# Performance work log

Hardware: AMD Instinct MI355X
Metric: run time of the kernel (lower is better)

Reference implementation:

```python
import jax, jax.numpy as jnp
import numpy as np

WS = 7
B, Dd, Hh, Wd, C, NH = 1, 28, 28, 28, 384, 12

def _rel_index(ws):
    coords = np.stack(np.meshgrid(np.arange(ws), np.arange(ws), np.arange(ws), indexing='ij'))
    cf = coords.reshape(3, -1)
    rel = (cf[:, :, None] - cf[:, None, :]).transpose(1, 2, 0) + (ws - 1)
    rel[:, :, 0] *= (2 * ws - 1) ** 2
    rel[:, :, 1] *= (2 * ws - 1)
    return rel.sum(-1)  # (ws^3, ws^3)

REL_IDX = _rel_index(WS)

def setup_inputs():
    key = jax.random.key(0)
    ks = jax.random.split(key, 8)
    L = Dd * Hh * Wd
    s = 0.02
    return {
        'skip': jax.random.normal(ks[0], (B, L, C), jnp.float32),
        'x_up': jax.random.normal(ks[1], (B, L, C), jnp.float32),
        'D': Dd, 'H': Hh, 'W': Wd,
        'ln1_g': jnp.ones((C,), jnp.float32), 'ln1_b': jnp.zeros((C,), jnp.float32),
        'kv_w': jax.random.normal(ks[2], (C, 2 * C), jnp.float32) * s,
        'kv_b': jnp.zeros((2 * C,), jnp.float32),
        'rpb': jax.random.normal(ks[3], ((2 * WS - 1) ** 3, NH), jnp.float32) * s,
        'proj_w': jax.random.normal(ks[4], (C, C), jnp.float32) * s,
        'proj_b': jnp.zeros((C,), jnp.float32),
        'ln2_g': jnp.ones((C,), jnp.float32), 'ln2_b': jnp.zeros((C,), jnp.float32),
        'mlp_w1': jax.random.normal(ks[5], (C, 4 * C), jnp.float32) * s,
        'mlp_b1': jnp.zeros((4 * C,), jnp.float32),
        'mlp_w2': jax.random.normal(ks[6], (4 * C, C), jnp.float32) * s,
        'mlp_b2': jnp.zeros((C,), jnp.float32),
    }

def _ln(x, g, b):
    m = jnp.mean(x, -1, keepdims=True)
    v = jnp.mean(jnp.square(x - m), -1, keepdims=True)
    return (x - m) * jax.lax.rsqrt(v + 1e-5) * g + b

def _win_part(x):
    b, d, h, w, c = x.shape
    x = x.reshape(b, d // WS, WS, h // WS, WS, w // WS, WS, c)
    return x.transpose(0, 1, 3, 5, 2, 4, 6, 7).reshape(-1, WS ** 3, c)

def _win_rev(x, b, d, h, w):
    c = x.shape[-1]
    x = x.reshape(b, d // WS, h // WS, w // WS, WS, WS, WS, c)
    return x.transpose(0, 1, 4, 2, 5, 3, 6, 7).reshape(b, d, h, w, c)

def reference(skip, x_up, D, H, W, ln1_g, ln1_b, kv_w, kv_b, rpb, proj_w, proj_b, ln2_g, ln2_b, mlp_w1, mlp_b1, mlp_w2, mlp_b2):
    b, L, c = skip.shape
    x = x_up + skip  # wrapper residual; shortcut of the inner block
    # inner block was built with shift_size=0 -> no cyclic shift, attn_mask unused
    sk = _win_part(_ln(skip, ln1_g, ln1_b).reshape(b, D, H, W, c))   # (nW, N, C) -> K,V source
    qx = _win_part(_ln(x_up, ln1_g, ln1_b).reshape(b, D, H, W, c))   # (nW, N, C) -> Q source
    nW, N, _ = sk.shape
    hd = c // NH
    kv = (sk @ kv_w + kv_b).reshape(nW, N, 2, NH, hd)
    k, v = kv[:, :, 0], kv[:, :, 1]                  # (nW, N, NH, hd)
    q = qx.reshape(nW, N, NH, hd) * (hd ** -0.5)     # no q projection in WindowAttention_kv
    attn = jnp.einsum('wqhd,wkhd->whqk', q, k)
    bias = rpb[REL_IDX.reshape(-1)].reshape(N, N, NH).transpose(2, 0, 1)
    attn = jax.nn.softmax(attn + bias[None], axis=-1)
    o = jnp.einsum('whqk,wkhd->wqhd', attn, v).reshape(nW, N, c)
    o = o @ proj_w + proj_b
    o = _win_rev(o, b, D, H, W).reshape(b, L, c)
    x = x + o
    h1 = jax.nn.gelu(_ln(x, ln2_g, ln2_b) @ mlp_w1 + mlp_b1)
    x = x + h1 @ mlp_w2 + mlp_b2
    return x
```

## Files before the change

### kernel.cpp

```cpp
#include <hip/hip_runtime.h>
#include <hip/hip_bf16.h>
#include <cstdint>

typedef unsigned short u16;
typedef short s16x8 __attribute__((ext_vector_type(8)));
typedef short s16x4 __attribute__((ext_vector_type(4)));
typedef float f32x4 __attribute__((ext_vector_type(4)));

#define C_DIM 384
#define NHEAD 12
#define HD    32
#define NTOK  343
#define NWIN  64
#define LTOT  21952
#define SIDE  28

__device__ __forceinline__ float u2f(u16 u) {
    return __uint_as_float(((unsigned int)u) << 16);
}
__device__ __forceinline__ u16 f2b(float f) {
    unsigned int u = __float_as_uint(f);
    return (u16)((u + 0x7fffu + ((u >> 16) & 1u)) >> 16);
}
__device__ __forceinline__ float exp2_hw(float x) {
    float r;
    asm("v_exp_f32 %0, %1" : "=v"(r) : "v"(x));
    return r;
}
__device__ __forceinline__ unsigned int pk_bf16(float lo, float hi) {
    unsigned int r;
    asm("v_cvt_pk_bf16_f32 %0, %1, %2" : "=v"(r) : "v"(lo), "v"(hi));
    return r;
}
__device__ __forceinline__ float gelu_fast(float x) {
    float e = exp2_hw(-2.3022083f * (x + 0.044715f * x * x * x));
    return x * __builtin_amdgcn_rcpf(1.f + e);
}

__global__ __launch_bounds__(256) void k_wt(
    const float* __restrict__ W, u16* __restrict__ Wt, int K, int N)
{
    __shared__ float T[64][65];
    int k0 = blockIdx.x * 64, n0 = blockIdx.y * 64;
    int t = threadIdx.x;
    int c = t & 63, rg = t >> 6;
#pragma unroll
    for (int i = 0; i < 16; i++) {
        int r = rg * 16 + i;
        T[r][c] = W[(size_t)(k0 + r) * N + n0 + c];
    }
    __syncthreads();
    int k = t & 63, ng = t >> 6;
#pragma unroll
    for (int i = 0; i < 16; i++) {
        int n = ng * 16 + i;
        Wt[(size_t)(n0 + n) * K + k0 + k] = f2b(T[k][n]);
    }
}

__global__ __launch_bounds__(256) void k_wt_pi(
    const float* __restrict__ W, u16* __restrict__ Wt, int K, int N)
{
    __shared__ float T[64][65];
    int k0 = blockIdx.x * 64, n0 = blockIdx.y * 64;
    int t = threadIdx.x;
    int c = t & 63, rg = t >> 6;
#pragma unroll
    for (int i = 0; i < 16; i++) {
        int r = rg * 16 + i;
        T[r][c] = W[(size_t)(k0 + r) * N + n0 + c];
    }
    __syncthreads();
    int k = t & 63, ng = t >> 6;
    int kg = k0 + k;
    int j = kg & 127, ct = j >> 4, nn = j & 15;
    int kp = (kg & ~127) | ((ct >> 1) << 5) | (nn << 1) | (ct & 1);
#pragma unroll
    for (int i = 0; i < 16; i++) {
        int n = ng * 16 + i;
        Wt[(size_t)(n0 + n) * K + kp] = f2b(T[k][n]);
    }
}

__global__ __launch_bounds__(256) void k_lnprep(
    const float* __restrict__ skip, const float* __restrict__ xup,
    const float* __restrict__ g, const float* __restrict__ bta,
    u16* __restrict__ skW, u16* __restrict__ qW, u16* __restrict__ res)
{
    int t = blockIdx.x * 4 + (threadIdx.x >> 6);
    int lane = threadIdx.x & 63;
    const float* ps = skip + (size_t)t * C_DIM;
    const float* px = xup + (size_t)t * C_DIM;
    float vs[6], vx[6];
    float s1 = 0.f, s2 = 0.f, x1 = 0.f, x2 = 0.f;
#pragma unroll
    for (int j = 0; j < 6; j++) {
        float a = ps[lane + j * 64];
        float b = px[lane + j * 64];
        vs[j] = a; vx[j] = b;
        s1 += a; s2 += a * a; x1 += b; x2 += b * b;
    }
#pragma unroll
    for (int off = 32; off; off >>= 1) {
        s1 += __shfl_xor(s1, off);
        s2 += __shfl_xor(s2, off);
        x1 += __shfl_xor(x1, off);
        x2 += __shfl_xor(x2, off);
    }
    float ms = s1 * (1.f / 384.f), mx = x1 * (1.f / 384.f);
    float rs = rsqrtf(fmaxf(s2 * (1.f / 384.f) - ms * ms, 0.f) + 1e-5f);
    float rx = rsqrtf(fmaxf(x2 * (1.f / 384.f) - mx * mx, 0.f) + 1e-5f);
    int d = t / 784, rem = t % 784, hh = rem / 28, ww = rem % 28;
    int win = (d / 7) * 16 + (hh / 7) * 4 + (ww / 7);
    int n = (d % 7) * 49 + (hh % 7) * 7 + (ww % 7);
    size_t dst = ((size_t)(win * NTOK + n)) * C_DIM + lane;
    size_t td  = (size_t)t * C_DIM + lane;
#pragma unroll
    for (int j = 0; j < 6; j++) {
        int c = lane + j * 64;
        float gg = g[c], bb = bta[c];
        skW[dst + j * 64] = f2b((vs[j] - ms) * rs * gg + bb);
        qW[dst + j * 64]  = f2b((vx[j] - mx) * rx * gg + bb);
        res[td + j * 64]  = f2b(vs[j] + vx[j]);
    }
}

__global__ __launch_bounds__(256) void k_ln2(
    const u16* __restrict__ x2, const float* __restrict__ g,
    const float* __restrict__ bta, u16* __restrict__ lnx)
{
    int t = blockIdx.x * 4 + (threadIdx.x >> 6);
    int lane = threadIdx.x & 63;
    const u16* p = x2 + (size_t)t * C_DIM;
    float v[6];
    float s1 = 0.f, s2 = 0.f;
#pragma unroll
    for (int j = 0; j < 6; j++) {
        float a = u2f(p[lane + j * 64]);
        v[j] = a; s1 += a; s2 += a * a;
    }
#pragma unroll
    for (int off = 32; off; off >>= 1) {
        s1 += __shfl_xor(s1, off);
        s2 += __shfl_xor(s2, off);
    }
    float m = s1 * (1.f / 384.f);
    float r = rsqrtf(fmaxf(s2 * (1.f / 384.f) - m * m, 0.f) + 1e-5f);
    size_t dst = (size_t)t * C_DIM + lane;
#pragma unroll
    for (int j = 0; j < 6; j++) {
        int c = lane + j * 64;
        lnx[dst + j * 64] = f2b((v[j] - m) * r * g[c] + bta[c]);
    }
}

#define BPAD 40

__device__ __forceinline__ void gemm128(
    const u16* __restrict__ A, const u16* __restrict__ Bt, int K, int M,
    int rowBase, int colBase, int tid,
    u16 (*As)[BPAD], u16 (*Bs)[BPAD], f32x4 acc[2][8])
{
    const int sr  = tid >> 2;
    const int scg = (tid & 3) << 3;
    const int lane = tid & 63, wv = tid >> 6;
    const int m16 = lane & 15, quad = lane >> 4;

    int ra0 = min(rowBase + sr, M - 1);
    int ra1 = min(rowBase + 64 + sr, M - 1);
    const u16* pa0 = A + (size_t)ra0 * K + scg;
    const u16* pa1 = A + (size_t)ra1 * K + scg;
    const u16* pb0 = Bt + (size_t)(colBase + sr) * K + scg;
    const u16* pb1 = Bt + (size_t)(colBase + 64 + sr) * K + scg;

    uint4 a0 = *(const uint4*)pa0, a1 = *(const uint4*)pa1;
    uint4 b0 = *(const uint4*)pb0, b1 = *(const uint4*)pb1;

    for (int kk = 0; kk < K; kk += 32) {
        *(uint4*)&As[sr][scg]      = a0;
        *(uint4*)&As[64 + sr][scg] = a1;
        *(uint4*)&Bs[sr][scg]      = b0;
        *(uint4*)&Bs[64 + sr][scg] = b1;
        __syncthreads();
        if (kk + 32 < K) {
            a0 = *(const uint4*)(pa0 + kk + 32);
            a1 = *(const uint4*)(pa1 + kk + 32);
            b0 = *(const uint4*)(pb0 + kk + 32);
            b1 = *(const uint4*)(pb1 + kk + 32);
        }
        s16x8 af0 = *(const s16x8*)&As[wv * 32 + m16][quad * 8];
        s16x8 af1 = *(const s16x8*)&As[wv * 32 + 16 + m16][quad * 8];
#pragma unroll
        for (int c = 0; c < 8; c++) {
            s16x8 bf = *(const s16x8*)&Bs[c * 16 + m16][quad * 8];
            acc[0][c] = __builtin_amdgcn_mfma_f32_16x16x32_bf16(af0, bf, acc[0][c], 0, 0, 0);
            acc[1][c] = __builtin_amdgcn_mfma_f32_16x16x32_bf16(af1, bf, acc[1][c], 0, 0, 0);
        }
        __syncthreads();
    }
}

__device__ __forceinline__ void gemm64_d2(
    const u16* __restrict__ A, const u16* __restrict__ Bt, int K, int M,
    int rowBase, int colBase, int tid,
    u16 (*As)[BPAD], u16 (*Bs)[BPAD], f32x4 acc[8])
{
    const int sr  = tid >> 2;
    const int scg = (tid & 3) << 3;
    const int lane = tid & 63, wv = tid >> 6;
    const int m16 = lane & 15, quad = lane >> 4;

    int ra = min(rowBase + sr, M - 1);
    const u16* pa  = A + (size_t)ra * K + scg;
    const u16* pb0 = Bt + (size_t)(colBase + sr) * K + scg;
    const u16* pb1 = Bt + (size_t)(colBase + 64 + sr) * K + scg;

    uint4 a0  = *(const uint4*)pa;
    uint4 b00 = *(const uint4*)pb0;
    uint4 b01 = *(const uint4*)pb1;
    uint4 a1  = *(const uint4*)(pa + 32);
    uint4 b10 = *(const uint4*)(pb0 + 32);
    uint4 b11 = *(const uint4*)(pb1 + 32);

    for (int kk = 0; kk < K; kk += 64) {
        *(uint4*)&As[sr][scg]      = a0;
        *(uint4*)&Bs[sr][scg]      = b00;
        *(uint4*)&Bs[64 + sr][scg] = b01;
        __syncthreads();
        if (kk + 64 < K) {
            a0  = *(const uint4*)(pa  + kk + 64);
            b00 = *(const uint4*)(pb0 + kk + 64);
            b01 = *(const uint4*)(pb1 + kk + 64);
        }
        {
            s16x8 af = *(const s16x8*)&As[wv * 16 + m16][quad * 8];
#pragma unroll
            for (int c = 0; c < 8; c++) {
                s16x8 bf = *(const s16x8*)&Bs[c * 16 + m16][quad * 8];
                acc[c] = __builtin_amdgcn_mfma_f32_16x16x32_bf16(af, bf, acc[c], 0, 0, 0);
            }
        }
        __syncthreads();
        *(uint4*)&As[sr][scg]      = a1;
        *(uint4*)&Bs[sr][scg]      = b10;
        *(uint4*)&Bs[64 + sr][scg] = b11;
        __syncthreads();
        if (kk + 96 < K) {
            a1  = *(const uint4*)(pa  + kk + 96);
            b10 = *(const uint4*)(pb0 + kk + 96);
            b11 = *(const uint4*)(pb1 + kk + 96);
        }
        {
            s16x8 af = *(const s16x8*)&As[wv * 16 + m16][quad * 8];
#pragma unroll
            for (int c = 0; c < 8; c++) {
                s16x8 bf = *(const s16x8*)&Bs[c * 16 + m16][quad * 8];
                acc[c] = __builtin_amdgcn_mfma_f32_16x16x32_bf16(af, bf, acc[c], 0, 0, 0);
            }
        }
        __syncthreads();
    }
}

#define EPI_SETUP \
    int lane = tid & 63, wv = tid >> 6, quad = lane >> 4, n16 = lane & 15;

__global__ __launch_bounds__(256) void k_gemm_kv(
    const u16* __restrict__ A, const u16* __restrict__ Wt, const float* __restrict__ bias,
    u16* __restrict__ Kb, u16* __restrict__ Vb)
{
    __shared__ __align__(16) u16 As[128][BPAD];
    __shared__ __align__(16) u16 Bs[128][BPAD];
    f32x4 acc[2][8] = {};
    int tid = threadIdx.x;
    int rowBase = blockIdx.x * 128, colBase = blockIdx.y * 128;
    gemm128(A, Wt, 384, LTOT, rowBase, colBase, tid, As, Bs, acc);
    EPI_SETUP
#pragma unroll
    for (int c = 0; c < 8; c++) {
        int col = colBase + c * 16 + n16;
        float bcol = bias[col];
        int isv = col >= 384;
        int remc = col - (isv ? 384 : 0);
        int hh = remc >> 5, dd = remc & 31;
#pragma unroll
        for (int rt = 0; rt < 2; rt++)
#pragma unroll
        for (int reg = 0; reg < 4; reg++) {
            int r = rowBase + wv * 32 + rt * 16 + quad * 4 + reg;
            if (r < LTOT) {
                int w = r / NTOK, nn = r % NTOK;
                size_t dst = ((size_t)((w * NHEAD + hh) * NTOK + nn)) * HD + dd;
                (isv ? Vb : Kb)[dst] = f2b(acc[rt][c][reg] + bcol);
            }
        }
    }
}

__global__ __launch_bounds__(256) void k_gemm_proj(
    const u16* __restrict__ A, const u16* __restrict__ Wt, const float* __restrict__ bias,
    const u16* __restrict__ res, u16* __restrict__ x2)
{
    __shared__ __align__(16) u16 As[64][BPAD];
    __shared__ __align__(16) u16 Bs[128][BPAD];
    f32x4 acc[8] = {};
    int tid = threadIdx.x;
    int rowBase = blockIdx.x * 64, colBase = blockIdx.y * 128;
    gemm64_d2(A, Wt, 384, LTOT, rowBase, colBase, tid, As, Bs, acc);
    EPI_SETUP
#pragma unroll
    for (int c = 0; c < 8; c++) {
        int col = colBase + c * 16 + n16;
        float bcol = bias[col];
#pragma unroll
        for (int reg = 0; reg < 4; reg++) {
            int r = rowBase + wv * 16 + quad * 4 + reg;
            if (r < LTOT) {
                size_t idx = (size_t)r * C_DIM + col;
                x2[idx] = f2b(acc[c][reg] + bcol + u2f(res[idx]));
            }
        }
    }
}

__global__ __launch_bounds__(256) void k_gemm_mlp1(
    const u16* __restrict__ A, const u16* __restrict__ Wt, const float* __restrict__ bias,
    u16* __restrict__ h1c, int rowOfs)
{
    __shared__ __align__(16) u16 As[128][BPAD];
    __shared__ __align__(16) u16 Bs[128][BPAD];
    f32x4 acc[2][8] = {};
    int tid = threadIdx.x;
    int rowBase = rowOfs + blockIdx.x * 128, colBase = blockIdx.y * 128;
    gemm128(A, Wt, 384, LTOT, rowBase, colBase, tid, As, Bs, acc);
    EPI_SETUP
#pragma unroll
    for (int p = 0; p < 4; p++) {
        int col0 = colBase + p * 32 + n16;
        int col1 = col0 + 16;
        float bc0 = bias[col0], bc1 = bias[col1];
        int dcol = colBase + p * 32 + 2 * n16;
#pragma unroll
        for (int rt = 0; rt < 2; rt++)
#pragma unroll
        for (int reg = 0; reg < 4; reg++) {
            int r = rowBase + wv * 32 + rt * 16 + quad * 4 + reg;
            if (r < LTOT) {
                size_t rl = (size_t)(r - rowOfs);
                float v0 = gelu_fast(acc[rt][2 * p][reg] + bc0);
                float v1 = gelu_fast(acc[rt][2 * p + 1][reg] + bc1);
                *(unsigned int*)&h1c[rl * 1536 + dcol] = pk_bf16(v0, v1);
            }
        }
    }
}

__global__ __launch_bounds__(256) void k_gemm_mlp2(
    const u16* __restrict__ A, const u16* __restrict__ Wt, const float* __restrict__ bias,
    const u16* __restrict__ x2, float* __restrict__ out, int rowOfs, int chunkRows)
{
    __shared__ __align__(16) u16 As[64][BPAD];
    __shared__ __align__(16) u16 Bs[128][BPAD];
    f32x4 acc[8] = {};
    int tid = threadIdx.x;
    int rowBase = blockIdx.x * 64, colBase = blockIdx.y * 128;
    gemm64_d2(A, Wt, 1536, chunkRows, rowBase, colBase, tid, As, Bs, acc);
    EPI_SETUP
#pragma unroll
    for (int c = 0; c < 8; c++) {
        int col = colBase + c * 16 + n16;
        float bcol = bias[col];
#pragma unroll
        for (int reg = 0; reg < 4; reg++) {
            int rl = rowBase + wv * 16 + quad * 4 + reg;
            int rg = rowOfs + rl;
            if (rl < chunkRows && rg < LTOT) {
                size_t idx = (size_t)rg * C_DIM + col;
                out[idx] = acc[c][reg] + bcol + u2f(x2[idx]);
            }
        }
    }
}

#define KP  40
#define VP  360
#define PBS 36

__global__ __launch_bounds__(256, 2) void k_attn(
    const u16* __restrict__ qW, const u16* __restrict__ Kb, const u16* __restrict__ Vb,
    const float* __restrict__ rpb, u16* __restrict__ oT)
{
    __shared__ __align__(16) u16 Ks[352 * KP];
    __shared__ __align__(16) u16 Vt[32 * VP];
    __shared__ __align__(16) u16 rp16[2200];
    __shared__ __align__(16) u16 code[352];
    __shared__ __align__(16) u16 Pb[4 * 16 * PBS];

    const int h = blockIdx.x, w = blockIdx.y;
    const int tid = threadIdx.x;
    const int lane = tid & 63, wv = tid >> 6;
    const int m16 = lane & 15, quad = lane >> 4;
    const size_t base = ((size_t)(w * NHEAD + h)) * NTOK * HD;

    for (int t = tid; t < 1408; t += 256) {
        int r = t >> 2, c = (t & 3) << 3;
        uint4 u = make_uint4(0, 0, 0, 0);
        if (r < NTOK) u = *(const uint4*)(Kb + base + r * HD + c);
        *(uint4*)&Ks[r * KP + c] = u;
    }
    for (int t = tid; t < 704; t += 256) {
        int dg = t / 176, rem = t - dg * 176;
        int kb = rem >> 4, j = rem & 15;
        int n0 = kb * 32 + j, n1 = n0 + 16;
        uint4 uA = make_uint4(0, 0, 0, 0), uB = make_uint4(0, 0, 0, 0);
        if (n0 < NTOK) uA = *(const uint4*)(Vb + base + n0 * HD + dg * 8);
        if (n1 < NTOK) uB = *(const uint4*)(Vb + base + n1 * HD + dg * 8);
        int d0 = dg * 8, colu = kb * 32 + 2 * j;
        unsigned int pk0 = (uA.x & 0xffffu) | (uB.x << 16);
        unsigned int pk1 = (uA.x >> 16)     | (uB.x & 0xffff0000u);
        unsigned int pk2 = (uA.y & 0xffffu) | (uB.y << 16);
        unsigned int pk3 = (uA.y >> 16)     | (uB.y & 0xffff0000u);
        unsigned int pk4 = (uA.z & 0xffffu) | (uB.z << 16);
        unsigned int pk5 = (uA.z >> 16)     | (uB.z & 0xffff0000u);
        unsigned int pk6 = (uA.w & 0xffffu) | (uB.w << 16);
        unsigned int pk7 = (uA.w >> 16)     | (uB.w & 0xffff0000u);
        *(unsigned int*)&Vt[(d0 + 0) * VP + colu] = pk0;
        *(unsigned int*)&Vt[(d0 + 1) * VP + colu] = pk1;
        *(unsigned int*)&Vt[(d0 + 2) * VP + colu] = pk2;
        *(unsigned int*)&Vt[(d0 + 3) * VP + colu] = pk3;
        *(unsigned int*)&Vt[(d0 + 4) * VP + colu] = pk4;
        *(unsigned int*)&Vt[(d0 + 5) * VP + colu] = pk5;
        *(unsigned int*)&Vt[(d0 + 6) * VP + colu] = pk6;
        *(unsigned int*)&Vt[(d0 + 7) * VP + colu] = pk7;
    }
    for (int t = tid; t < 2200; t += 256)
        rp16[t] = (t < 2197) ? f2b(rpb[t * NHEAD + h] * 1.4426950408889634f) : (u16)0;
    for (int t = tid; t < 352; t += 256) {
        int z = t / 49, rem = t % 49, y = rem / 7, x = rem % 7;
        code[t] = (t < NTOK) ? (u16)(z * 169 + y * 13 + x) : (u16)1098;
    }
    __syncthreads();

    const float scale = 0.2550348772f;
    u16* myP = Pb + wv * 16 * PBS;

    for (int qt = wv; qt < 22; qt += 4) {
        int qbase = qt * 16;
        int qrow = min(qbase + m16, NTOK - 1);
        s16x8 qf = *(const s16x8*)(qW + ((size_t)(w * NTOK + qrow)) * C_DIM
                                       + h * HD + quad * 8);
        int qcv[4];
#pragma unroll
        for (int i = 0; i < 4; i++) qcv[i] = code[qbase + quad * 4 + i];

        f32x4 S0[11], S1[11];
        float mx[4] = {-1e30f, -1e30f, -1e30f, -1e30f};

#pragma unroll
        for (int ks = 0; ks < 11; ks++) {
            int kbase = ks * 32;
            int kt0 = kbase + m16, kt1 = kt0 + 16;
            s16x8 kf0 = *(const s16x8*)&Ks[kt0 * KP + quad * 8];
            s16x8 kf1 = *(const s16x8*)&Ks[kt1 * KP + quad * 8];
            f32x4 z = {0.f, 0.f, 0.f, 0.f};
            f32x4 sA = __builtin_amdgcn_mfma_f32_16x16x32_bf16(qf, kf0, z, 0, 0, 0);
            f32x4 sB = __builtin_amdgcn_mfma_f32_16x16x32_bf16(qf, kf1, z, 0, 0, 0);
            int kc0 = code[kt0], kc1 = code[kt1];
            bool k1ok = (ks < 10) || (kt1 < NTOK);
#pragma unroll
            for (int i = 0; i < 4; i++) {
                float b0 = u2f(rp16[qcv[i] - kc0 + 1098]);
                float b1 = u2f(rp16[qcv[i] - kc1 + 1098]);
                float sa = fmaf(sA[i], scale, b0);
                float sb = k1ok ? fmaf(sB[i], scale, b1) : -1e30f;
                S0[ks][i] = sa;
                S1[ks][i] = sb;
                mx[i] = fmaxf(mx[i], fmaxf(sa, sb));
            }
        }
#pragma unroll
        for (int i = 0; i < 4; i++) {
            float v = mx[i];
            v = fmaxf(v, __shfl_xor(v, 1));
            v = fmaxf(v, __shfl_xor(v, 2));
            v = fmaxf(v, __shfl_xor(v, 4));
            v = fmaxf(v, __shfl_xor(v, 8));
            mx[i] = v;
        }

        f32x4 O0 = {}, O1 = {};
        float l[4] = {};
#pragma unroll
        for (int ks = 0; ks < 11; ks++) {
            int kbase = ks * 32;
#pragma unroll
            for (int i = 0; i < 4; i++) {
                float pa = exp2_hw(S0[ks][i] - mx[i]);
                float pb = exp2_hw(S1[ks][i] - mx[i]);
                l[i] += pa + pb;
                *(unsigned int*)&myP[(quad * 4 + i) * PBS + 2 * m16] = pk_bf16(pa, pb);
            }
            s16x4 plo = *(const s16x4*)&myP[m16 * PBS + quad * 8];
            s16x4 phi = *(const s16x4*)&myP[m16 * PBS + quad * 8 + 4];
            s16x8 pf  = __builtin_shufflevector(plo, phi, 0, 1, 2, 3, 4, 5, 6, 7);
            s16x8 vf0 = *(const s16x8*)&Vt[m16 * VP + kbase + quad * 8];
            s16x8 vf1 = *(const s16x8*)&Vt[(16 + m16) * VP + kbase + quad * 8];
            O0 = __builtin_amdgcn_mfma_f32_16x16x32_bf16(pf, vf0, O0, 0, 0, 0);
            O1 = __builtin_amdgcn_mfma_f32_16x16x32_bf16(pf, vf1, O1, 0, 0, 0);
        }
#pragma unroll
        for (int i = 0; i < 4; i++) {
            float v = l[i];
            v += __shfl_xor(v, 1);
            v += __shfl_xor(v, 2);
            v += __shfl_xor(v, 4);
            v += __shfl_xor(v, 8);
            l[i] = v;
        }

        int wd = w >> 4, wh = (w >> 2) & 3, wwi = w & 3;
#pragma unroll
        for (int i = 0; i < 4; i++) {
            int q = qbase + quad * 4 + i;
            if (q < NTOK) {
                float rl = __builtin_amdgcn_rcpf(l[i]);
                int qz = q / 49, qrem = q % 49, qy = qrem / 7, qx = qrem % 7;
                size_t tok = ((size_t)(wd * 7 + qz) * SIDE + (wh * 7 + qy)) * SIDE
                             + (wwi * 7 + qx);
                u16* op = oT + tok * C_DIM + h * HD;
                op[m16]      = f2b(O0[i] * rl);
                op[16 + m16] = f2b(O1[i] * rl);
            }
        }
    }
}

extern "C" void kernel_launch(void* const* d_in, const int* in_sizes, int n_in,
                              void* d_out, int out_size, void* d_ws, size_t ws_size,
                              hipStream_t stream)
{
    const float* skip = (const float*)d_in[0];
    const float* xup  = (const float*)d_in[1];
    const float* ln1g = (const float*)d_in[5];
    const float* ln1b = (const float*)d_in[6];
    const float* kvw  = (const float*)d_in[7];
    const float* kvb  = (const float*)d_in[8];
    const float* rpb  = (const float*)d_in[9];
    const float* pw   = (const float*)d_in[10];
    const float* pb   = (const float*)d_in[11];
    const float* ln2g = (const float*)d_in[12];
    const float* ln2b = (const float*)d_in[13];
    const float* w1   = (const float*)d_in[14];
    const float* b1   = (const float*)d_in[15];
    const float* w2   = (const float*)d_in[16];
    const float* b2   = (const float*)d_in[17];
    float* out = (float*)d_out;

    char* ws = (char*)d_ws;
    const size_t BUFB = (size_t)LTOT * C_DIM * 2;
    const size_t WTB  = 589824 + 294912 + 1179648 + 1179648;
    u16* skW = (u16*)(ws);
    u16* qW  = (u16*)(ws + BUFB);
    u16* Kb  = (u16*)(ws + 2 * BUFB);
    u16* Vb  = (u16*)(ws + 3 * BUFB);
    u16* oT  = (u16*)(ws);
    u16* x2  = (u16*)(ws + BUFB);
    u16* lnx = (u16*)(ws + 2 * BUFB);
    char* wt = ws + 4 * BUFB;
    u16* kvWt = (u16*)(wt);
    u16* pWt  = (u16*)(wt + 589824);
    u16* w1t  = (u16*)(wt + 589824 + 294912);
    u16* w2t  = (u16*)(wt + 589824 + 294912 + 1179648);
    u16* res  = (u16*)d_out;

    const size_t used = 4 * BUFB + WTB;
    const size_t blkBytes = 128 * 1536 * 2;
    size_t tailCap = (ws_size > used) ? (ws_size - used) / blkBytes : 0;
    int chunkBlocks;
    u16* h1c;
    if (tailCap >= 43) {
        chunkBlocks = tailCap < 172 ? (int)tailCap : 172;
        h1c = (u16*)(ws + used);
    } else {
        chunkBlocks = 42;
        h1c = (u16*)(ws + 3 * BUFB);
    }

    k_wt<<<dim3(6, 12), 256, 0, stream>>>(kvw, kvWt, 384, 768);
    k_wt<<<dim3(6, 6),  256, 0, stream>>>(pw,  pWt,  384, 384);
    k_wt<<<dim3(6, 24), 256, 0, stream>>>(w1,  w1t,  384, 1536);
    k_wt_pi<<<dim3(24, 6), 256, 0, stream>>>(w2, w2t, 1536, 384);

    k_lnprep<<<LTOT / 4, 256, 0, stream>>>(skip, xup, ln1g, ln1b, skW, qW, res);
    k_gemm_kv<<<dim3(172, 6), 256, 0, stream>>>(skW, kvWt, kvb, Kb, Vb);
    k_attn<<<dim3(NHEAD, NWIN), 256, 0, stream>>>(qW, Kb, Vb, rpb, oT);
    k_gemm_proj<<<dim3(343, 3), 256, 0, stream>>>(oT, pWt, pb, res, x2);
    k_ln2<<<LTOT / 4, 256, 0, stream>>>(x2, ln2g, ln2b, lnx);
    for (int b0 = 0; b0 < 172; b0 += chunkBlocks) {
        int nb = (172 - b0) < chunkBlocks ? (172 - b0) : chunkBlocks;
        int rowOfs = b0 * 128;
        int chunkRows = nb * 128;
        if (rowOfs + chunkRows > LTOT) chunkRows = LTOT - rowOfs;
        int nb64 = (chunkRows + 63) / 64;
        k_gemm_mlp1<<<dim3(nb, 12), 256, 0, stream>>>(lnx, w1t, b1, h1c, rowOfs);
        k_gemm_mlp2<<<dim3(nb64, 3), 256, 0, stream>>>(h1c, w2t, b2, x2, out, rowOfs, chunkRows);
    }
}
```

Measured before the change: 421.0 us.

## Use 2x2 warp tiling in GEMMs and double-buffer LDS for 64-row GEMMs

The 128x128 GEMM now gives each wave a 64x64 quadrant instead of a 32x128 strip. That drops per-wave LDS fragment reads from 10 to 8 for each k-step, since 4 A plus 4 B fragments are shared across 16 MFMAs. The 64-row GEMM used by proj and mlp2 now splits waves along N (32 columns each, all 64 rows) and uses two LDS buffers, so each 32-wide k slice needs one barrier instead of two. In exchange, LDS use doubles for proj/mlp2 and epilogue store patterns change, which may affect coalescing and occupancy.

```diff
diff --git a/kernel.cpp b/kernel.cpp
--- a/kernel.cpp
+++ b/kernel.cpp
@@ -159,12 +159,13 @@
 __device__ __forceinline__ void gemm128(
     const u16* __restrict__ A, const u16* __restrict__ Bt, int K, int M,
     int rowBase, int colBase, int tid,
-    u16 (*As)[BPAD], u16 (*Bs)[BPAD], f32x4 acc[2][8])
+    u16 (*As)[BPAD], u16 (*Bs)[BPAD], f32x4 acc[4][4])
 {
     const int sr  = tid >> 2;
     const int scg = (tid & 3) << 3;
     const int lane = tid & 63, wv = tid >> 6;
     const int m16 = lane & 15, quad = lane >> 4;
+    const int wr = (wv >> 1) << 6, wc = (wv & 1) << 6;
 
     int ra0 = min(rowBase + sr, M - 1);
     int ra1 = min(rowBase + 64 + sr, M - 1);
@@ -188,75 +189,98 @@
             b0 = *(const uint4*)(pb0 + kk + 32);
             b1 = *(const uint4*)(pb1 + kk + 32);
         }
-        s16x8 af0 = *(const s16x8*)&As[wv * 32 + m16][quad * 8];
-        s16x8 af1 = *(const s16x8*)&As[wv * 32 + 16 + m16][quad * 8];
-#pragma unroll
-        for (int c = 0; c < 8; c++) {
-            s16x8 bf = *(const s16x8*)&Bs[c * 16 + m16][quad * 8];
-            acc[0][c] = __builtin_amdgcn_mfma_f32_16x16x32_bf16(af0, bf, acc[0][c], 0, 0, 0);
-            acc[1][c] = __builtin_amdgcn_mfma_f32_16x16x32_bf16(af1, bf, acc[1][c], 0, 0, 0);
-        }
+        s16x8 af[4], bf[4];
+#pragma unroll
+        for (int rt = 0; rt < 4; rt++)
+            af[rt] = *(const s16x8*)&As[wr + rt * 16 + m16][quad * 8];
+#pragma unroll
+        for (int bt = 0; bt < 4; bt++)
+            bf[bt] = *(const s16x8*)&Bs[wc + bt * 16 + m16][quad * 8];
+#pragma unroll
+        for (int rt = 0; rt < 4; rt++)
+#pragma unroll
+        for (int bt = 0; bt < 4; bt++)
+            acc[rt][bt] = __builtin_amdgcn_mfma_f32_16x16x32_bf16(af[rt], bf[bt], acc[rt][bt], 0, 0, 0);
         __syncthreads();
     }
 }
 
-__device__ __forceinline__ void gemm64_d2(
+__device__ __forceinline__ void gemm64_db(
     const u16* __restrict__ A, const u16* __restrict__ Bt, int K, int M,
     int rowBase, int colBase, int tid,
-    u16 (*As)[BPAD], u16 (*Bs)[BPAD], f32x4 acc[8])
+    u16 (*As)[BPAD], u16 (*Bs)[BPAD], f32x4 acc[4][2])
 {
     const int sr  = tid >> 2;
     const int scg = (tid & 3) << 3;
     const int lane = tid & 63, wv = tid >> 6;
     const int m16 = lane & 15, quad = lane >> 4;
+    const int wc = wv << 5;
 
     int ra = min(rowBase + sr, M - 1);
     const u16* pa  = A + (size_t)ra * K + scg;
     const u16* pb0 = Bt + (size_t)(colBase + sr) * K + scg;
     const u16* pb1 = Bt + (size_t)(colBase + 64 + sr) * K + scg;
 
-    uint4 a0  = *(const uint4*)pa;
-    uint4 b00 = *(const uint4*)pb0;
-    uint4 b01 = *(const uint4*)pb1;
-    uint4 a1  = *(const uint4*)(pa + 32);
-    uint4 b10 = *(const uint4*)(pb0 + 32);
-    uint4 b11 = *(const uint4*)(pb1 + 32);
+    uint4 aA = *(const uint4*)pa,        bA0 = *(const uint4*)pb0,        bA1 = *(const uint4*)pb1;
+    uint4 aB = *(const uint4*)(pa + 32), bB0 = *(const uint4*)(pb0 + 32), bB1 = *(const uint4*)(pb1 + 32);
+
+    *(uint4*)&As[sr][scg]      = aA;
+    *(uint4*)&Bs[sr][scg]      = bA0;
+    *(uint4*)&Bs[64 + sr][scg] = bA1;
+    if (64 < K) {
+        aA  = *(const uint4*)(pa + 64);
+        bA0 = *(const uint4*)(pb0 + 64);
+        bA1 = *(const uint4*)(pb1 + 64);
+    }
+    __syncthreads();
 
     for (int kk = 0; kk < K; kk += 64) {
-        *(uint4*)&As[sr][scg]      = a0;
-        *(uint4*)&Bs[sr][scg]      = b00;
-        *(uint4*)&Bs[64 + sr][scg] = b01;
+        *(uint4*)&As[64 + sr][scg]  = aB;
+        *(uint4*)&Bs[128 + sr][scg] = bB0;
+        *(uint4*)&Bs[192 + sr][scg] = bB1;
+        if (kk + 96 < K) {
+            aB  = *(const uint4*)(pa  + kk + 96);
+            bB0 = *(const uint4*)(pb0 + kk + 96);
+            bB1 = *(const uint4*)(pb1 + kk + 96);
+        }
+        {
+            s16x8 af[4], bf[2];
+#pragma unroll
+            for (int rt = 0; rt < 4; rt++)
+                af[rt] = *(const s16x8*)&As[rt * 16 + m16][quad * 8];
+#pragma unroll
+            for (int bt = 0; bt < 2; bt++)
+                bf[bt] = *(const s16x8*)&Bs[wc + bt * 16 + m16][quad * 8];
+#pragma unroll
+            for (int rt = 0; rt < 4; rt++)
+#pragma unroll
+            for (int bt = 0; bt < 2; bt++)
+                acc[rt][bt] = __builtin_amdgcn_mfma_f32_16x16x32_bf16(af[rt], bf[bt], acc[rt][bt], 0, 0, 0);
+        }
         __syncthreads();
         if (kk + 64 < K) {
-            a0  = *(const uint4*)(pa  + kk + 64);
-            b00 = *(const uint4*)(pb0 + kk + 64);
-            b01 = *(const uint4*)(pb1 + kk + 64);
+            *(uint4*)&As[sr][scg]      = aA;
+            *(uint4*)&Bs[sr][scg]      = bA0;
+            *(uint4*)&Bs[64 + sr][scg] = bA1;
+        }
+        if (kk + 128 < K) {
+            aA  = *(const uint4*)(pa  + kk + 128);
+            bA0 = *(const uint4*)(pb0 + kk + 128);
+            bA1 = *(const uint4*)(pb1 + kk + 128);
         }
         {
-            s16x8 af = *(const s16x8*)&As[wv * 16 + m16][quad * 8];
-#pragma unroll
-            for (int c = 0; c < 8; c++) {
-                s16x8 bf = *(const s16x8*)&Bs[c * 16 + m16][quad * 8];
-                acc[c] = __builtin_amdgcn_mfma_f32_16x16x32_bf16(af, bf, acc[c], 0, 0, 0);
-            }
-        }
-        __syncthreads();
-        *(uint4*)&As[sr][scg]      = a1;
-        *(uint4*)&Bs[sr][scg]      = b10;
-        *(uint4*)&Bs[64 + sr][scg] = b11;
-        __syncthreads();
-        if (kk + 96 < K) {
-            a1  = *(const uint4*)(pa  + kk + 96);
-            b10 = *(const uint4*)(pb0 + kk + 96);
-            b11 = *(const uint4*)(pb1 + kk + 96);
-        }
-        {
-            s16x8 af = *(const s16x8*)&As[wv * 16 + m16][quad * 8];
-#pragma unroll
-            for (int c = 0; c < 8; c++) {
-                s16x8 bf = *(const s16x8*)&Bs[c * 16 + m16][quad * 8];
-                acc[c] = __builtin_amdgcn_mfma_f32_16x16x32_bf16(af, bf, acc[c], 0, 0, 0);
-            }
+            s16x8 af[4], bf[2];
+#pragma unroll
+            for (int rt = 0; rt < 4; rt++)
+                af[rt] = *(const s16x8*)&As[64 + rt * 16 + m16][quad * 8];
+#pragma unroll
+            for (int bt = 0; bt < 2; bt++)
+                bf[bt] = *(const s16x8*)&Bs[128 + wc + bt * 16 + m16][quad * 8];
+#pragma unroll
+            for (int rt = 0; rt < 4; rt++)
+#pragma unroll
+            for (int bt = 0; bt < 2; bt++)
+                acc[rt][bt] = __builtin_amdgcn_mfma_f32_16x16x32_bf16(af[rt], bf[bt], acc[rt][bt], 0, 0, 0);
         }
         __syncthreads();
     }
@@ -271,27 +295,28 @@
 {
     __shared__ __align__(16) u16 As[128][BPAD];
     __shared__ __align__(16) u16 Bs[128][BPAD];
-    f32x4 acc[2][8] = {};
+    f32x4 acc[4][4] = {};
     int tid = threadIdx.x;
     int rowBase = blockIdx.x * 128, colBase = blockIdx.y * 128;
     gemm128(A, Wt, 384, LTOT, rowBase, colBase, tid, As, Bs, acc);
     EPI_SETUP
-#pragma unroll
-    for (int c = 0; c < 8; c++) {
-        int col = colBase + c * 16 + n16;
+    int wr = (wv >> 1) << 6, wc = (wv & 1) << 6;
+#pragma unroll
+    for (int bt = 0; bt < 4; bt++) {
+        int col = colBase + wc + bt * 16 + n16;
         float bcol = bias[col];
         int isv = col >= 384;
         int remc = col - (isv ? 384 : 0);
         int hh = remc >> 5, dd = remc & 31;
 #pragma unroll
-        for (int rt = 0; rt < 2; rt++)
+        for (int rt = 0; rt < 4; rt++)
 #pragma unroll
         for (int reg = 0; reg < 4; reg++) {
-            int r = rowBase + wv * 32 + rt * 16 + quad * 4 + reg;
+            int r = rowBase + wr + rt * 16 + quad * 4 + reg;
             if (r < LTOT) {
                 int w = r / NTOK, nn = r % NTOK;
                 size_t dst = ((size_t)((w * NHEAD + hh) * NTOK + nn)) * HD + dd;
-                (isv ? Vb : Kb)[dst] = f2b(acc[rt][c][reg] + bcol);
+                (isv ? Vb : Kb)[dst] = f2b(acc[rt][bt][reg] + bcol);
             }
         }
     }
@@ -301,23 +326,26 @@
     const u16* __restrict__ A, const u16* __restrict__ Wt, const float* __restrict__ bias,
     const u16* __restrict__ res, u16* __restrict__ x2)
 {
-    __shared__ __align__(16) u16 As[64][BPAD];
-    __shared__ __align__(16) u16 Bs[128][BPAD];
-    f32x4 acc[8] = {};
+    __shared__ __align__(16) u16 As[128][BPAD];
+    __shared__ __align__(16) u16 Bs[256][BPAD];
+    f32x4 acc[4][2] = {};
     int tid = threadIdx.x;
     int rowBase = blockIdx.x * 64, colBase = blockIdx.y * 128;
-    gemm64_d2(A, Wt, 384, LTOT, rowBase, colBase, tid, As, Bs, acc);
+    gemm64_db(A, Wt, 384, LTOT, rowBase, colBase, tid, As, Bs, acc);
     EPI_SETUP
-#pragma unroll
-    for (int c = 0; c < 8; c++) {
-        int col = colBase + c * 16 + n16;
+    int wc = wv << 5;
+#pragma unroll
+    for (int bt = 0; bt < 2; bt++) {
+        int col = colBase + wc + bt * 16 + n16;
         float bcol = bias[col];
 #pragma unroll
+        for (int rt = 0; rt < 4; rt++)
+#pragma unroll
         for (int reg = 0; reg < 4; reg++) {
-            int r = rowBase + wv * 16 + quad * 4 + reg;
+            int r = rowBase + rt * 16 + quad * 4 + reg;
             if (r < LTOT) {
                 size_t idx = (size_t)r * C_DIM + col;
-                x2[idx] = f2b(acc[c][reg] + bcol + u2f(res[idx]));
+                x2[idx] = f2b(acc[rt][bt][reg] + bcol + u2f(res[idx]));
             }
         }
     }
@@ -329,26 +357,28 @@
 {
     __shared__ __align__(16) u16 As[128][BPAD];
     __shared__ __align__(16) u16 Bs[128][BPAD];
-    f32x4 acc[2][8] = {};
+    f32x4 acc[4][4] = {};
     int tid = threadIdx.x;
     int rowBase = rowOfs + blockIdx.x * 128, colBase = blockIdx.y * 128;
     gemm128(A, Wt, 384, LTOT, rowBase, colBase, tid, As, Bs, acc);
     EPI_SETUP
-#pragma unroll
-    for (int p = 0; p < 4; p++) {
+    int wr = (wv >> 1) << 6;
+#pragma unroll
+    for (int p2 = 0; p2 < 2; p2++) {
+        int p = (wv & 1) * 2 + p2;
         int col0 = colBase + p * 32 + n16;
         int col1 = col0 + 16;
         float bc0 = bias[col0], bc1 = bias[col1];
         int dcol = colBase + p * 32 + 2 * n16;
 #pragma unroll
-        for (int rt = 0; rt < 2; rt++)
+        for (int rt = 0; rt < 4; rt++)
 #pragma unroll
         for (int reg = 0; reg < 4; reg++) {
-            int r = rowBase + wv * 32 + rt * 16 + quad * 4 + reg;
+            int r = rowBase + wr + rt * 16 + quad * 4 + reg;
             if (r < LTOT) {
                 size_t rl = (size_t)(r - rowOfs);
-                float v0 = gelu_fast(acc[rt][2 * p][reg] + bc0);
-                float v1 = gelu_fast(acc[rt][2 * p + 1][reg] + bc1);
+                float v0 = gelu_fast(acc[rt][2 * p2][reg] + bc0);
+                float v1 = gelu_fast(acc[rt][2 * p2 + 1][reg] + bc1);
                 *(unsigned int*)&h1c[rl * 1536 + dcol] = pk_bf16(v0, v1);
             }
         }
@@ -359,24 +389,27 @@
     const u16* __restrict__ A, const u16* __restrict__ Wt, const float* __restrict__ bias,
     const u16* __restrict__ x2, float* __restrict__ out, int rowOfs, int chunkRows)
 {
-    __shared__ __align__(16) u16 As[64][BPAD];
-    __shared__ __align__(16) u16 Bs[128][BPAD];
-    f32x4 acc[8] = {};
+    __shared__ __align__(16) u16 As[128][BPAD];
+    __shared__ __align__(16) u16 Bs[256][BPAD];
+    f32x4 acc[4][2] = {};
     int tid = threadIdx.x;
     int rowBase = blockIdx.x * 64, colBase = blockIdx.y * 128;
-    gemm64_d2(A, Wt, 1536, chunkRows, rowBase, colBase, tid, As, Bs, acc);
+    gemm64_db(A, Wt, 1536, chunkRows, rowBase, colBase, tid, As, Bs, acc);
     EPI_SETUP
-#pragma unroll
-    for (int c = 0; c < 8; c++) {
-        int col = colBase + c * 16 + n16;
+    int wc = wv << 5;
+#pragma unroll
+    for (int bt = 0; bt < 2; bt++) {
+        int col = colBase + wc + bt * 16 + n16;
         float bcol = bias[col];
 #pragma unroll
+        for (int rt = 0; rt < 4; rt++)
+#pragma unroll
         for (int reg = 0; reg < 4; reg++) {
-            int rl = rowBase + wv * 16 + quad * 4 + reg;
+            int rl = rowBase + rt * 16 + quad * 4 + reg;
             int rg = rowOfs + rl;
             if (rl < chunkRows && rg < LTOT) {
                 size_t idx = (size_t)rg * C_DIM + col;
-                out[idx] = acc[c][reg] + bcol + u2f(x2[idx]);
+                out[idx] = acc[rt][bt][reg] + bcol + u2f(x2[idx]);
             }
         }
     }
```

Result: slower. 432.2 us (+2.7%).
